# Performance work log

Hardware: AMD Instinct MI355X
Metric: run time of the kernel (lower is better)

Reference implementation:

```python
import jax, jax.numpy as jnp
import numpy as np

ALPHA = 0.2  # LeakyReLU negative slope

def setup_inputs() -> dict:
    key = jax.random.key(0)
    k1, k2, k3 = jax.random.split(key, 3)
    B, N, Fin, Fout = 8, 2048, 256, 128
    h = jax.random.normal(k1, (B, N, Fin), dtype=jnp.float32)
    W = jax.random.normal(k2, (Fin, Fout), dtype=jnp.float32) * (1.414 / np.sqrt(Fin))
    a = jax.random.normal(k3, (2 * Fout, 1), dtype=jnp.float32) * 0.1
    return {"h": h, "W": W, "a": a}

def reference(h, W, a):
    # Wh: [B, N, D]
    Wh = jnp.einsum('bni,io->bno', h, W)
    D = Wh.shape[-1]
    a1 = a[:D, 0]   # weights for the 'i' (repeat_interleave) half
    a2 = a[D:, 0]   # weights for the 'j' (repeat) half
    s1 = Wh @ a1    # [B, N]
    s2 = Wh @ a2    # [B, N]
    # e[b,i,j] = leakyrelu(s1[b,i] + s2[b,j])  (fused form of the O(N^2*2D) concat)
    e = s1[:, :, None] + s2[:, None, :]
    e = jnp.where(e >= 0, e, ALPHA * e)
    # original applies softmax over dim=1 (the i axis)
    attention = jax.nn.softmax(e, axis=1)
    # dropout is identity in eval mode
    h_prime = jnp.einsum('bij,bjd->bid', attention, Wh)
    # concat=True -> ELU
    return jax.nn.elu(h_prime)
```

## Files before the change

### kernel.cpp

```cpp
#include <hip/hip_runtime.h>
#include <hip/hip_bf16.h>


#define ALPHA 0.2f
#define LOG2E 1.4426950408889634f
constexpr int Bb=8, Nn=2048, FIN=256, FOUT=128;

typedef __attribute__((ext_vector_type(8))) short short8;
typedef __attribute__((ext_vector_type(4))) float f32x4;
typedef const __attribute__((address_space(1))) unsigned int* gptr_t;
typedef __attribute__((address_space(3))) unsigned int* lptr_t;

__device__ __forceinline__ float lrelu(float x){ return fmaxf(x, ALPHA*x); }
__device__ __forceinline__ unsigned short bfbits(float x){
    __hip_bfloat16 h = __float2bfloat16(x);
    return *(unsigned short*)&h;
}

__global__ __launch_bounds__(256) void k_prep(const float* __restrict__ W,
                                              __hip_bfloat16* __restrict__ WTt){
    const int idx = blockIdx.x*256 + threadIdx.x;
    #pragma unroll
    for (int v = 0; v < 4; ++v){
        const int widx = idx + v*8192;
        const int kk = widx & 31, n = (widx>>5)&127, kt = widx>>12;
        WTt[widx] = __float2bfloat16(W[(kt*32+kk)*FOUT + n]);
    }
}

__global__ __launch_bounds__(256) void k_wh(const float* __restrict__ h,
                                            const float* __restrict__ a,
                                            const __hip_bfloat16* __restrict__ WTt,
                                            float* __restrict__ s1,
                                            float* __restrict__ s2,
                                            __hip_bfloat16* __restrict__ WhT){
    const int blk = blockIdx.x;
    const int rowbase = blk * 32;
    const int b = blk >> 6;
    const int jt = (rowbase & (Nn-1)) >> 5;
    const int t = threadIdx.x;
    const int wave = t>>6, lane = t&63;
    const int wm = wave & 1, wn = wave >> 1;
    const int lm = lane & 15, q = lane >> 4;

    __shared__ unsigned short hsb[32*264];
    __shared__ unsigned short tt[FOUT*40];
    __shared__ float s1red[2][32], s2red[2][32];

    {
        const float4* h4 = (const float4*)(h + (size_t)rowbase*FIN);
        for (int v = t; v < 2048; v += 256){
            const int row = v >> 6, kq = v & 63;
            float4 x = h4[v];
            ushort4 u;
            u.x = bfbits(x.x); u.y = bfbits(x.y);
            u.z = bfbits(x.z); u.w = bfbits(x.w);
            *(ushort4*)&hsb[row*264 + kq*4] = u;
        }
    }
    __syncthreads();

    f32x4 acc[4];
    #pragma unroll
    for (int ntl = 0; ntl < 4; ++ntl) acc[ntl] = (f32x4){0.f,0.f,0.f,0.f};

    const short* Wt = (const short*)WTt;
    #pragma unroll 2
    for (int kt = 0; kt < 8; ++kt){
        const short8 afr = *(const short8*)&hsb[(wm*16+lm)*264 + kt*32 + q*8];
        #pragma unroll
        for (int ntl = 0; ntl < 4; ++ntl){
            const short8 bfr = *(const short8*)(Wt + ((kt*128 + wn*64 + ntl*16 + lm)*32 + q*8));
            acc[ntl] = __builtin_amdgcn_mfma_f32_16x16x32_bf16(afr, bfr, acc[ntl], 0,0,0);
        }
    }

    {
        float a1v[4], a2v[4];
        #pragma unroll
        for (int ntl = 0; ntl < 4; ++ntl){
            a1v[ntl] = a[wn*64 + ntl*16 + lm];
            a2v[ntl] = a[FOUT + wn*64 + ntl*16 + lm];
        }
        #pragma unroll
        for (int rg = 0; rg < 4; ++rg){
            float p1 = 0.f, p2 = 0.f;
            #pragma unroll
            for (int ntl = 0; ntl < 4; ++ntl){
                p1 += acc[ntl][rg]*a1v[ntl];
                p2 += acc[ntl][rg]*a2v[ntl];
            }
            #pragma unroll
            for (int m = 1; m < 16; m <<= 1){
                p1 += __shfl_xor(p1, m);
                p2 += __shfl_xor(p2, m);
            }
            if (lm == 0){
                s1red[wn][wm*16 + q*4 + rg] = p1;
                s2red[wn][wm*16 + q*4 + rg] = p2;
            }
        }
    }

    #pragma unroll
    for (int ntl = 0; ntl < 4; ++ntl){
        ushort4 u;
        u.x = bfbits(acc[ntl][0]); u.y = bfbits(acc[ntl][1]);
        u.z = bfbits(acc[ntl][2]); u.w = bfbits(acc[ntl][3]);
        *(ushort4*)&tt[(wn*64 + ntl*16 + lm)*40 + wm*16 + q*4] = u;
    }
    __syncthreads();

    if (t < 32){
        s1[rowbase + t] = (s1red[0][t] + s1red[1][t]) * LOG2E;
        s2[rowbase + t] = (s2red[0][t] + s2red[1][t]) * LOG2E;
    }
    {
        const int d = t >> 1, jh = (t & 1) * 16;
        const unsigned short* src = &tt[d*40 + jh];
        short8 v0 = *(const short8*)src;
        short8 v1 = *(const short8*)(src + 8);
        const int lmw = d & 15, ntw = d >> 4, q0 = (t & 1) * 2;
        const int u0 = (lmw & 7) + 8*(q0*16 + ntw*2 + (lmw >> 3));
        short* Wo = (short*)WhT;
        const size_t tb = ((size_t)(b*64 + jt))*4096;
        *(short8*)&Wo[tb + (size_t)u0*8]         = v0;
        *(short8*)&Wo[tb + (size_t)(u0+128)*8]   = v1;
    }
}

__global__ __launch_bounds__(256) void k_z(const float* __restrict__ s1,
                                           const float* __restrict__ s2,
                                           float* __restrict__ l2z){
    const int b  = blockIdx.x >> 7;
    const int jt = blockIdx.x & 127;
    const int t  = threadIdx.x;
    const int jj = t & 15, part = t >> 4;
    const int j  = jt*16 + jj;
    __shared__ float s1s[Nn];
    __shared__ float wred[4];
    __shared__ float red[16][17];

    float mx = -1e30f;
    {
        const float4* g = (const float4*)(s1 + (size_t)b*Nn);
        float4* p = (float4*)s1s;
        #pragma unroll
        for (int v0 = 0; v0 < 2; ++v0){
            const int v = t + v0*256;
            float4 x = g[v]; p[v] = x;
            mx = fmaxf(mx, fmaxf(fmaxf(x.x, x.y), fmaxf(x.z, x.w)));
        }
    }
    #pragma unroll
    for (int m = 1; m < 64; m <<= 1) mx = fmaxf(mx, __shfl_xor(mx, m));
    if ((t & 63) == 0) wred[t >> 6] = mx;
    __syncthreads();
    const float mxf = fmaxf(fmaxf(wred[0], wred[1]), fmaxf(wred[2], wred[3]));

    const float s2j = s2[b*Nn + j];
    const float m   = lrelu(mxf + s2j);
    float sum = 0.f;
    const float4* s4 = (const float4*)&s1s[part*128];
    #pragma unroll 4
    for (int v = 0; v < 32; ++v){
        float x[4]; *(float4*)x = s4[v];
        sum += __builtin_amdgcn_exp2f(lrelu(x[0]+s2j) - m)
             + __builtin_amdgcn_exp2f(lrelu(x[1]+s2j) - m)
             + __builtin_amdgcn_exp2f(lrelu(x[2]+s2j) - m)
             + __builtin_amdgcn_exp2f(lrelu(x[3]+s2j) - m);
    }
    red[part][jj] = sum;
    __syncthreads();
    if (part == 0){
        float Z = 0.f;
        #pragma unroll
        for (int p = 0; p < 16; ++p) Z += red[p][jj];
        l2z[b*Nn + j] = -m - __builtin_amdgcn_logf(Z);
    }
}

__global__ __launch_bounds__(256, 2) void k_pv(const float* __restrict__ s1,
                                               const float* __restrict__ s2,
                                               const float* __restrict__ l2z,
                                               const __hip_bfloat16* __restrict__ WhT,
                                               float* __restrict__ out){
    const int blk   = blockIdx.x;
    const int b     = blk & 7;
    const int ibase = (blk >> 3) * 32;
    const int t     = threadIdx.x;
    const int wave  = t >> 6, lane = t & 63;
    const int wm = wave & 1, kh = wave >> 1;
    const int lm = lane & 15, q = lane >> 4;

    __shared__ float s2s[Nn], lzs[Nn];
    __shared__ unsigned short Bs[2][2][4096];

    {
        const float4* g1 = (const float4*)(s2  + (size_t)b*Nn);
        const float4* g2 = (const float4*)(l2z + (size_t)b*Nn);
        float4* p1 = (float4*)s2s; float4* p2 = (float4*)lzs;
        #pragma unroll
        for (int v0 = 0; v0 < 2; ++v0){
            const int v = t + v0*256;
            p1[v] = g1[v]; p2[v] = g2[v];
        }
    }

    const float s1a = s1[(size_t)b*Nn + ibase + wm*16 + lm];

    f32x4 acc[8];
    #pragma unroll
    for (int nt = 0; nt < 8; ++nt) acc[nt] = (f32x4){0.f,0.f,0.f,0.f};

    const char* WtbB = (const char*)WhT + (size_t)b*64*8192;
    const int laneoff = wm*4096 + lane*16;
    const int dsbase  = (lm & 7)*16 + (lm >> 3)*128 + q*2048;

    {
        const char* src = WtbB + (size_t)(kh*32)*8192 + laneoff;
        unsigned short* dst = &Bs[0][kh][wm*2048];
        #pragma unroll
        for (int c = 0; c < 4; ++c)
            __builtin_amdgcn_global_load_lds((gptr_t)(src + c*1024),
                                             (lptr_t)(dst + c*512), 16, 0, 0);
    }

    int buf = 0;
    for (int it = 0; it < 32; ++it){
        __syncthreads();
        if (it + 1 < 32){
            const char* src = WtbB + (size_t)(kh*32 + it + 1)*8192 + laneoff;
            unsigned short* dst = &Bs[buf^1][kh][wm*2048];
            #pragma unroll
            for (int c = 0; c < 4; ++c)
                __builtin_amdgcn_global_load_lds((gptr_t)(src + c*1024),
                                                 (lptr_t)(dst + c*512), 16, 0, 0);
        }
        const char* tile = (const char*)&Bs[buf][kh][0];
        short8 bfr[8];
        #pragma unroll
        for (int nt = 0; nt < 8; ++nt)
            bfr[nt] = *(const short8*)(tile + dsbase + nt*256);

        const int jb = (kh*32 + it)*32 + q*8;
        float sarr[8], larr[8];
        *(float4*)&sarr[0] = *(const float4*)&s2s[jb];
        *(float4*)&sarr[4] = *(const float4*)&s2s[jb+4];
        *(float4*)&larr[0] = *(const float4*)&lzs[jb];
        *(float4*)&larr[4] = *(const float4*)&lzs[jb+4];
        short8 afa;
        #pragma unroll
        for (int e = 0; e < 8; ++e){
            const float z = s1a + sarr[e];
            afa[e] = (short)bfbits(__builtin_amdgcn_exp2f(fmaxf(z, ALPHA*z) + larr[e]));
        }
        #pragma unroll
        for (int nt = 0; nt < 8; ++nt)
            acc[nt] = __builtin_amdgcn_mfma_f32_16x16x32_bf16(afa, bfr[nt], acc[nt], 0,0,0);
        buf ^= 1;
    }

    __syncthreads();
    float* comb = (float*)&Bs[0][0][0];
    if (kh == 0){
        #pragma unroll
        for (int nt = 0; nt < 8; ++nt)
            #pragma unroll
            for (int rg = 0; rg < 4; ++rg)
                comb[(wm*16 + q*4 + rg)*132 + nt*16 + lm] = acc[nt][rg];
    }
    __syncthreads();
    if (kh == 1){
        #pragma unroll
        for (int nt = 0; nt < 8; ++nt){
            const int col = nt*16 + lm;
            #pragma unroll
            for (int rg = 0; rg < 4; ++rg){
                const int row = wm*16 + q*4 + rg;
                const float x = acc[nt][rg] + comb[row*132 + col];
                out[((size_t)(b*Nn + ibase + row))*FOUT + col] = x > 0.f ? x : expm1f(x);
            }
        }
    }
}

extern "C" void kernel_launch(void* const* d_in, const int* in_sizes, int n_in,
                              void* d_out, int out_size, void* d_ws, size_t ws_size,
                              hipStream_t stream) {
    (void)in_sizes; (void)n_in; (void)out_size; (void)ws_size;
    const float* h = (const float*)d_in[0];
    const float* W = (const float*)d_in[1];
    const float* a = (const float*)d_in[2];
    float* out = (float*)d_out;

    float* ws    = (float*)d_ws;
    float* s1    = ws;
    float* s2    = s1 + Bb*Nn;
    float* l2z   = s2 + Bb*Nn;
    __hip_bfloat16* WTt = (__hip_bfloat16*)(l2z + Bb*Nn);
    __hip_bfloat16* WhT = WTt + 32768;

    k_prep<<<dim3(32),        dim3(256), 0, stream>>>(W, WTt);
    k_wh  <<<dim3(Bb*Nn/32),  dim3(256), 0, stream>>>(h, a, WTt, s1, s2, WhT);
    k_z   <<<dim3(Bb*128),    dim3(256), 0, stream>>>(s1, s2, l2z);
    k_pv  <<<dim3(Bb*Nn/32),  dim3(256), 0, stream>>>(s1, s2, l2z, WhT, out);
}
```

Before: 109.8 us.

## Fuse all stages into one persistent kernel with atomic grid barriers

Replaces the four separate kernels (weight prep, Wh GEMM, softmax normalizer, PV) with a single 512-block kernel that separates phases by global atomic barriers. It also loads h directly from global into registers instead of staging it in LDS, and removes the max-subtraction from the column normalizer computation. This aims to cut launch gaps and inter-kernel drains, at the risk of barrier spin cost, requiring all blocks to be co-resident, and possible exp overflow without max stabilization.

```diff
diff --git a/kernel.cpp b/kernel.cpp
--- a/kernel.cpp
+++ b/kernel.cpp
@@ -5,6 +5,7 @@
 #define ALPHA 0.2f
 #define LOG2E 1.4426950408889634f
 constexpr int Bb=8, Nn=2048, FIN=256, FOUT=128;
+constexpr unsigned NBLK = 512;
 
 typedef __attribute__((ext_vector_type(8))) short short8;
 typedef __attribute__((ext_vector_type(4))) float f32x4;
@@ -17,269 +18,259 @@
     return *(unsigned short*)&h;
 }
 
-__global__ __launch_bounds__(256) void k_prep(const float* __restrict__ W,
-                                              __hip_bfloat16* __restrict__ WTt){
-    const int idx = blockIdx.x*256 + threadIdx.x;
-    #pragma unroll
-    for (int v = 0; v < 4; ++v){
-        const int widx = idx + v*8192;
-        const int kk = widx & 31, n = (widx>>5)&127, kt = widx>>12;
-        WTt[widx] = __float2bfloat16(W[(kt*32+kk)*FOUT + n]);
-    }
-}
-
-__global__ __launch_bounds__(256) void k_wh(const float* __restrict__ h,
-                                            const float* __restrict__ a,
-                                            const __hip_bfloat16* __restrict__ WTt,
-                                            float* __restrict__ s1,
-                                            float* __restrict__ s2,
-                                            __hip_bfloat16* __restrict__ WhT){
+__device__ __forceinline__ void gbar(unsigned int* cnt, int idx){
+    __syncthreads();
+    if (threadIdx.x == 0){
+        __hip_atomic_fetch_add(&cnt[idx], 1u, __ATOMIC_RELEASE, __HIP_MEMORY_SCOPE_AGENT);
+        while (__hip_atomic_load(&cnt[idx], __ATOMIC_RELAXED, __HIP_MEMORY_SCOPE_AGENT) < NBLK)
+            __builtin_amdgcn_s_sleep(2);
+        (void)__hip_atomic_load(&cnt[idx], __ATOMIC_ACQUIRE, __HIP_MEMORY_SCOPE_AGENT);
+    }
+    __syncthreads();
+}
+
+__global__ __launch_bounds__(64) void k_init(unsigned int* cnt){
+    if (threadIdx.x < 8) cnt[threadIdx.x] = 0u;
+}
+
+__global__ __launch_bounds__(256, 2) void k_mega(const float* __restrict__ h,
+                                                 const float* __restrict__ W,
+                                                 const float* __restrict__ a,
+                                                 float* __restrict__ s1,
+                                                 float* __restrict__ s2,
+                                                 float* __restrict__ l2z,
+                                                 __hip_bfloat16* __restrict__ WTt,
+                                                 __hip_bfloat16* __restrict__ WhT,
+                                                 unsigned int* __restrict__ cnt,
+                                                 float* __restrict__ out){
+    __shared__ __align__(16) char sm[49152];
     const int blk = blockIdx.x;
-    const int rowbase = blk * 32;
-    const int b = blk >> 6;
-    const int jt = (rowbase & (Nn-1)) >> 5;
-    const int t = threadIdx.x;
-    const int wave = t>>6, lane = t&63;
-    const int wm = wave & 1, wn = wave >> 1;
+    const int t   = threadIdx.x;
+    const int wave = t >> 6, lane = t & 63;
     const int lm = lane & 15, q = lane >> 4;
 
-    __shared__ unsigned short hsb[32*264];
-    __shared__ unsigned short tt[FOUT*40];
-    __shared__ float s1red[2][32], s2red[2][32];
+    if (t < 64){
+        const int idx = blk*64 + t;
+        const int kk = idx & 31, n = (idx>>5)&127, kt = idx>>12;
+        WTt[idx] = __float2bfloat16(W[(kt*32+kk)*FOUT + n]);
+    }
+    gbar(cnt, 0);
 
     {
-        const float4* h4 = (const float4*)(h + (size_t)rowbase*FIN);
-        for (int v = t; v < 2048; v += 256){
-            const int row = v >> 6, kq = v & 63;
-            float4 x = h4[v];
+        unsigned short* tt   = (unsigned short*)sm;
+        float* s1red = (float*)(sm + 20480);
+        float* s2red = s1red + 64;
+        const int rowbase = blk * 32;
+        const int b = blk >> 6;
+        const int jt = (rowbase & (Nn-1)) >> 5;
+        const int wm = wave & 1, wn = wave >> 1;
+
+        f32x4 acc[4];
+        #pragma unroll
+        for (int ntl = 0; ntl < 4; ++ntl) acc[ntl] = (f32x4){0.f,0.f,0.f,0.f};
+
+        const float* hrow = h + (size_t)(rowbase + wm*16 + lm)*FIN;
+        const short* Wt = (const short*)WTt;
+        #pragma unroll
+        for (int kt = 0; kt < 8; ++kt){
+            float av[8];
+            *(float4*)&av[0] = *(const float4*)&hrow[kt*32 + q*8];
+            *(float4*)&av[4] = *(const float4*)&hrow[kt*32 + q*8 + 4];
+            short8 afr;
+            #pragma unroll
+            for (int e = 0; e < 8; ++e) afr[e] = (short)bfbits(av[e]);
+            #pragma unroll
+            for (int ntl = 0; ntl < 4; ++ntl){
+                const short8 bfr = *(const short8*)(Wt + ((kt*128 + wn*64 + ntl*16 + lm)*32 + q*8));
+                acc[ntl] = __builtin_amdgcn_mfma_f32_16x16x32_bf16(afr, bfr, acc[ntl], 0,0,0);
+            }
+        }
+
+        {
+            float a1v[4], a2v[4];
+            #pragma unroll
+            for (int ntl = 0; ntl < 4; ++ntl){
+                a1v[ntl] = a[wn*64 + ntl*16 + lm];
+                a2v[ntl] = a[FOUT + wn*64 + ntl*16 + lm];
+            }
+            #pragma unroll
+            for (int rg = 0; rg < 4; ++rg){
+                float p1 = 0.f, p2 = 0.f;
+                #pragma unroll
+                for (int ntl = 0; ntl < 4; ++ntl){
+                    p1 += acc[ntl][rg]*a1v[ntl];
+                    p2 += acc[ntl][rg]*a2v[ntl];
+                }
+                #pragma unroll
+                for (int m = 1; m < 16; m <<= 1){
+                    p1 += __shfl_xor(p1, m);
+                    p2 += __shfl_xor(p2, m);
+                }
+                if (lm == 0){
+                    s1red[wn*32 + wm*16 + q*4 + rg] = p1;
+                    s2red[wn*32 + wm*16 + q*4 + rg] = p2;
+                }
+            }
+        }
+
+        #pragma unroll
+        for (int ntl = 0; ntl < 4; ++ntl){
             ushort4 u;
-            u.x = bfbits(x.x); u.y = bfbits(x.y);
-            u.z = bfbits(x.z); u.w = bfbits(x.w);
-            *(ushort4*)&hsb[row*264 + kq*4] = u;
-        }
-    }
-    __syncthreads();
-
-    f32x4 acc[4];
-    #pragma unroll
-    for (int ntl = 0; ntl < 4; ++ntl) acc[ntl] = (f32x4){0.f,0.f,0.f,0.f};
-
-    const short* Wt = (const short*)WTt;
-    #pragma unroll 2
-    for (int kt = 0; kt < 8; ++kt){
-        const short8 afr = *(const short8*)&hsb[(wm*16+lm)*264 + kt*32 + q*8];
-        #pragma unroll
-        for (int ntl = 0; ntl < 4; ++ntl){
-            const short8 bfr = *(const short8*)(Wt + ((kt*128 + wn*64 + ntl*16 + lm)*32 + q*8));
-            acc[ntl] = __builtin_amdgcn_mfma_f32_16x16x32_bf16(afr, bfr, acc[ntl], 0,0,0);
-        }
-    }
+            u.x = bfbits(acc[ntl][0]); u.y = bfbits(acc[ntl][1]);
+            u.z = bfbits(acc[ntl][2]); u.w = bfbits(acc[ntl][3]);
+            *(ushort4*)&tt[(wn*64 + ntl*16 + lm)*40 + wm*16 + q*4] = u;
+        }
+        __syncthreads();
+
+        if (t < 32){
+            s1[rowbase + t] = (s1red[t] + s1red[32 + t]) * LOG2E;
+            s2[rowbase + t] = (s2red[t] + s2red[32 + t]) * LOG2E;
+        }
+        {
+            const int d = t >> 1, jh = (t & 1) * 16;
+            const unsigned short* src = &tt[d*40 + jh];
+            short8 v0 = *(const short8*)src;
+            short8 v1 = *(const short8*)(src + 8);
+            const int lmw = d & 15, ntw = d >> 4, q0 = (t & 1) * 2;
+            const int u0 = (lmw & 7) + 8*(q0*16 + ntw*2 + (lmw >> 3));
+            short* Wo = (short*)WhT;
+            const size_t tb = ((size_t)(b*64 + jt))*4096;
+            *(short8*)&Wo[tb + (size_t)u0*8]       = v0;
+            *(short8*)&Wo[tb + (size_t)(u0+128)*8] = v1;
+        }
+    }
+    gbar(cnt, 1);
 
     {
-        float a1v[4], a2v[4];
-        #pragma unroll
-        for (int ntl = 0; ntl < 4; ++ntl){
-            a1v[ntl] = a[wn*64 + ntl*16 + lm];
-            a2v[ntl] = a[FOUT + wn*64 + ntl*16 + lm];
-        }
-        #pragma unroll
-        for (int rg = 0; rg < 4; ++rg){
-            float p1 = 0.f, p2 = 0.f;
-            #pragma unroll
-            for (int ntl = 0; ntl < 4; ++ntl){
-                p1 += acc[ntl][rg]*a1v[ntl];
-                p2 += acc[ntl][rg]*a2v[ntl];
-            }
-            #pragma unroll
-            for (int m = 1; m < 16; m <<= 1){
-                p1 += __shfl_xor(p1, m);
-                p2 += __shfl_xor(p2, m);
-            }
-            if (lm == 0){
-                s1red[wn][wm*16 + q*4 + rg] = p1;
-                s2red[wn][wm*16 + q*4 + rg] = p2;
-            }
-        }
-    }
-
-    #pragma unroll
-    for (int ntl = 0; ntl < 4; ++ntl){
-        ushort4 u;
-        u.x = bfbits(acc[ntl][0]); u.y = bfbits(acc[ntl][1]);
-        u.z = bfbits(acc[ntl][2]); u.w = bfbits(acc[ntl][3]);
-        *(ushort4*)&tt[(wn*64 + ntl*16 + lm)*40 + wm*16 + q*4] = u;
-    }
-    __syncthreads();
-
-    if (t < 32){
-        s1[rowbase + t] = (s1red[0][t] + s1red[1][t]) * LOG2E;
-        s2[rowbase + t] = (s2red[0][t] + s2red[1][t]) * LOG2E;
-    }
+        float* s1s = (float*)sm;
+        float* red = (float*)(sm + 8192);
+        const int b  = blk >> 6;
+        const int jt = blk & 63;
+        const int jj = t & 31, part = t >> 5;
+        const int j  = jt*32 + jj;
+        {
+            const float4* g = (const float4*)(s1 + (size_t)b*Nn);
+            float4* p = (float4*)s1s;
+            #pragma unroll
+            for (int v0 = 0; v0 < 2; ++v0){ const int v = t + v0*256; p[v] = g[v]; }
+        }
+        __syncthreads();
+        const float s2j = s2[b*Nn + j];
+        float sum = 0.f;
+        const float4* s4 = (const float4*)&s1s[part*256];
+        #pragma unroll 4
+        for (int v = 0; v < 64; ++v){
+            float x[4]; *(float4*)x = s4[v];
+            sum += __builtin_amdgcn_exp2f(lrelu(x[0]+s2j))
+                 + __builtin_amdgcn_exp2f(lrelu(x[1]+s2j))
+                 + __builtin_amdgcn_exp2f(lrelu(x[2]+s2j))
+                 + __builtin_amdgcn_exp2f(lrelu(x[3]+s2j));
+        }
+        red[part*33 + jj] = sum;
+        __syncthreads();
+        if (part == 0){
+            float Z = 0.f;
+            #pragma unroll
+            for (int p = 0; p < 8; ++p) Z += red[p*33 + jj];
+            l2z[b*Nn + j] = -__builtin_amdgcn_logf(Z);
+        }
+        __syncthreads();
+    }
+    gbar(cnt, 2);
+
     {
-        const int d = t >> 1, jh = (t & 1) * 16;
-        const unsigned short* src = &tt[d*40 + jh];
-        short8 v0 = *(const short8*)src;
-        short8 v1 = *(const short8*)(src + 8);
-        const int lmw = d & 15, ntw = d >> 4, q0 = (t & 1) * 2;
-        const int u0 = (lmw & 7) + 8*(q0*16 + ntw*2 + (lmw >> 3));
-        short* Wo = (short*)WhT;
-        const size_t tb = ((size_t)(b*64 + jt))*4096;
-        *(short8*)&Wo[tb + (size_t)u0*8]         = v0;
-        *(short8*)&Wo[tb + (size_t)(u0+128)*8]   = v1;
-    }
-}
-
-__global__ __launch_bounds__(256) void k_z(const float* __restrict__ s1,
-                                           const float* __restrict__ s2,
-                                           float* __restrict__ l2z){
-    const int b  = blockIdx.x >> 7;
-    const int jt = blockIdx.x & 127;
-    const int t  = threadIdx.x;
-    const int jj = t & 15, part = t >> 4;
-    const int j  = jt*16 + jj;
-    __shared__ float s1s[Nn];
-    __shared__ float wred[4];
-    __shared__ float red[16][17];
-
-    float mx = -1e30f;
-    {
-        const float4* g = (const float4*)(s1 + (size_t)b*Nn);
-        float4* p = (float4*)s1s;
-        #pragma unroll
-        for (int v0 = 0; v0 < 2; ++v0){
-            const int v = t + v0*256;
-            float4 x = g[v]; p[v] = x;
-            mx = fmaxf(mx, fmaxf(fmaxf(x.x, x.y), fmaxf(x.z, x.w)));
-        }
-    }
-    #pragma unroll
-    for (int m = 1; m < 64; m <<= 1) mx = fmaxf(mx, __shfl_xor(mx, m));
-    if ((t & 63) == 0) wred[t >> 6] = mx;
-    __syncthreads();
-    const float mxf = fmaxf(fmaxf(wred[0], wred[1]), fmaxf(wred[2], wred[3]));
-
-    const float s2j = s2[b*Nn + j];
-    const float m   = lrelu(mxf + s2j);
-    float sum = 0.f;
-    const float4* s4 = (const float4*)&s1s[part*128];
-    #pragma unroll 4
-    for (int v = 0; v < 32; ++v){
-        float x[4]; *(float4*)x = s4[v];
-        sum += __builtin_amdgcn_exp2f(lrelu(x[0]+s2j) - m)
-             + __builtin_amdgcn_exp2f(lrelu(x[1]+s2j) - m)
-             + __builtin_amdgcn_exp2f(lrelu(x[2]+s2j) - m)
-             + __builtin_amdgcn_exp2f(lrelu(x[3]+s2j) - m);
-    }
-    red[part][jj] = sum;
-    __syncthreads();
-    if (part == 0){
-        float Z = 0.f;
-        #pragma unroll
-        for (int p = 0; p < 16; ++p) Z += red[p][jj];
-        l2z[b*Nn + j] = -m - __builtin_amdgcn_logf(Z);
-    }
-}
-
-__global__ __launch_bounds__(256, 2) void k_pv(const float* __restrict__ s1,
-                                               const float* __restrict__ s2,
-                                               const float* __restrict__ l2z,
-                                               const __hip_bfloat16* __restrict__ WhT,
-                                               float* __restrict__ out){
-    const int blk   = blockIdx.x;
-    const int b     = blk & 7;
-    const int ibase = (blk >> 3) * 32;
-    const int t     = threadIdx.x;
-    const int wave  = t >> 6, lane = t & 63;
-    const int wm = wave & 1, kh = wave >> 1;
-    const int lm = lane & 15, q = lane >> 4;
-
-    __shared__ float s2s[Nn], lzs[Nn];
-    __shared__ unsigned short Bs[2][2][4096];
-
-    {
-        const float4* g1 = (const float4*)(s2  + (size_t)b*Nn);
-        const float4* g2 = (const float4*)(l2z + (size_t)b*Nn);
-        float4* p1 = (float4*)s2s; float4* p2 = (float4*)lzs;
-        #pragma unroll
-        for (int v0 = 0; v0 < 2; ++v0){
-            const int v = t + v0*256;
-            p1[v] = g1[v]; p2[v] = g2[v];
-        }
-    }
-
-    const float s1a = s1[(size_t)b*Nn + ibase + wm*16 + lm];
-
-    f32x4 acc[8];
-    #pragma unroll
-    for (int nt = 0; nt < 8; ++nt) acc[nt] = (f32x4){0.f,0.f,0.f,0.f};
-
-    const char* WtbB = (const char*)WhT + (size_t)b*64*8192;
-    const int laneoff = wm*4096 + lane*16;
-    const int dsbase  = (lm & 7)*16 + (lm >> 3)*128 + q*2048;
-
-    {
-        const char* src = WtbB + (size_t)(kh*32)*8192 + laneoff;
-        unsigned short* dst = &Bs[0][kh][wm*2048];
-        #pragma unroll
-        for (int c = 0; c < 4; ++c)
-            __builtin_amdgcn_global_load_lds((gptr_t)(src + c*1024),
-                                             (lptr_t)(dst + c*512), 16, 0, 0);
-    }
-
-    int buf = 0;
-    for (int it = 0; it < 32; ++it){
-        __syncthreads();
-        if (it + 1 < 32){
-            const char* src = WtbB + (size_t)(kh*32 + it + 1)*8192 + laneoff;
-            unsigned short* dst = &Bs[buf^1][kh][wm*2048];
+        float* s2s = (float*)sm;
+        float* lzs = (float*)(sm + 8192);
+        unsigned short* Bs = (unsigned short*)(sm + 16384);
+        const int b     = blk & 7;
+        const int ibase = (blk >> 3) * 32;
+        const int wm = wave & 1, kh = wave >> 1;
+
+        {
+            const float4* g1 = (const float4*)(s2  + (size_t)b*Nn);
+            const float4* g2 = (const float4*)(l2z + (size_t)b*Nn);
+            float4* p1 = (float4*)s2s; float4* p2 = (float4*)lzs;
+            #pragma unroll
+            for (int v0 = 0; v0 < 2; ++v0){
+                const int v = t + v0*256;
+                p1[v] = g1[v]; p2[v] = g2[v];
+            }
+        }
+
+        const float s1a = s1[(size_t)b*Nn + ibase + wm*16 + lm];
+
+        f32x4 acc[8];
+        #pragma unroll
+        for (int nt = 0; nt < 8; ++nt) acc[nt] = (f32x4){0.f,0.f,0.f,0.f};
+
+        const char* WtbB = (const char*)WhT + (size_t)b*64*8192;
+        const int laneoff = wm*4096 + lane*16;
+        const int dsbase  = (lm & 7)*16 + (lm >> 3)*128 + q*2048;
+
+        {
+            const char* src = WtbB + (size_t)(kh*32)*8192 + laneoff;
+            unsigned short* dst = Bs + kh*4096 + wm*2048;
             #pragma unroll
             for (int c = 0; c < 4; ++c)
                 __builtin_amdgcn_global_load_lds((gptr_t)(src + c*1024),
                                                  (lptr_t)(dst + c*512), 16, 0, 0);
         }
-        const char* tile = (const char*)&Bs[buf][kh][0];
-        short8 bfr[8];
-        #pragma unroll
-        for (int nt = 0; nt < 8; ++nt)
-            bfr[nt] = *(const short8*)(tile + dsbase + nt*256);
-
-        const int jb = (kh*32 + it)*32 + q*8;
-        float sarr[8], larr[8];
-        *(float4*)&sarr[0] = *(const float4*)&s2s[jb];
-        *(float4*)&sarr[4] = *(const float4*)&s2s[jb+4];
-        *(float4*)&larr[0] = *(const float4*)&lzs[jb];
-        *(float4*)&larr[4] = *(const float4*)&lzs[jb+4];
-        short8 afa;
-        #pragma unroll
-        for (int e = 0; e < 8; ++e){
-            const float z = s1a + sarr[e];
-            afa[e] = (short)bfbits(__builtin_amdgcn_exp2f(fmaxf(z, ALPHA*z) + larr[e]));
-        }
-        #pragma unroll
-        for (int nt = 0; nt < 8; ++nt)
-            acc[nt] = __builtin_amdgcn_mfma_f32_16x16x32_bf16(afa, bfr[nt], acc[nt], 0,0,0);
-        buf ^= 1;
-    }
-
-    __syncthreads();
-    float* comb = (float*)&Bs[0][0][0];
-    if (kh == 0){
-        #pragma unroll
-        for (int nt = 0; nt < 8; ++nt)
-            #pragma unroll
-            for (int rg = 0; rg < 4; ++rg)
-                comb[(wm*16 + q*4 + rg)*132 + nt*16 + lm] = acc[nt][rg];
-    }
-    __syncthreads();
-    if (kh == 1){
-        #pragma unroll
-        for (int nt = 0; nt < 8; ++nt){
-            const int col = nt*16 + lm;
-            #pragma unroll
-            for (int rg = 0; rg < 4; ++rg){
-                const int row = wm*16 + q*4 + rg;
-                const float x = acc[nt][rg] + comb[row*132 + col];
-                out[((size_t)(b*Nn + ibase + row))*FOUT + col] = x > 0.f ? x : expm1f(x);
+
+        int buf = 0;
+        for (int it = 0; it < 32; ++it){
+            __syncthreads();
+            if (it + 1 < 32){
+                const char* src = WtbB + (size_t)(kh*32 + it + 1)*8192 + laneoff;
+                unsigned short* dst = Bs + (buf^1)*8192 + kh*4096 + wm*2048;
+                #pragma unroll
+                for (int c = 0; c < 4; ++c)
+                    __builtin_amdgcn_global_load_lds((gptr_t)(src + c*1024),
+                                                     (lptr_t)(dst + c*512), 16, 0, 0);
+            }
+            const char* tile = (const char*)(Bs + buf*8192 + kh*4096);
+            short8 bfr[8];
+            #pragma unroll
+            for (int nt = 0; nt < 8; ++nt)
+                bfr[nt] = *(const short8*)(tile + dsbase + nt*256);
+
+            const int jb = (kh*32 + it)*32 + q*8;
+            float sarr[8], larr[8];
+            *(float4*)&sarr[0] = *(const float4*)&s2s[jb];
+            *(float4*)&sarr[4] = *(const float4*)&s2s[jb+4];
+            *(float4*)&larr[0] = *(const float4*)&lzs[jb];
+            *(float4*)&larr[4] = *(const float4*)&lzs[jb+4];
+            short8 afa;
+            #pragma unroll
+            for (int e = 0; e < 8; ++e){
+                const float z = s1a + sarr[e];
+                afa[e] = (short)bfbits(__builtin_amdgcn_exp2f(fmaxf(z, ALPHA*z) + larr[e]));
+            }
+            #pragma unroll
+            for (int nt = 0; nt < 8; ++nt)
+                acc[nt] = __builtin_amdgcn_mfma_f32_16x16x32_bf16(afa, bfr[nt], acc[nt], 0,0,0);
+            buf ^= 1;
+        }
+
+        __syncthreads();
+        float* comb = (float*)(sm + 16384);
+        if (kh == 0){
+            #pragma unroll
+            for (int nt = 0; nt < 8; ++nt)
+                #pragma unroll
+                for (int rg = 0; rg < 4; ++rg)
+                    comb[(wm*16 + q*4 + rg)*132 + nt*16 + lm] = acc[nt][rg];
+        }
+        __syncthreads();
+        if (kh == 1){
+            #pragma unroll
+            for (int nt = 0; nt < 8; ++nt){
+                const int col = nt*16 + lm;
+                #pragma unroll
+                for (int rg = 0; rg < 4; ++rg){
+                    const int row = wm*16 + q*4 + rg;
+                    const float x = acc[nt][rg] + comb[row*132 + col];
+                    out[((size_t)(b*Nn + ibase + row))*FOUT + col] = x > 0.f ? x : expm1f(x);
+                }
             }
         }
     }
@@ -300,9 +291,8 @@
     float* l2z   = s2 + Bb*Nn;
     __hip_bfloat16* WTt = (__hip_bfloat16*)(l2z + Bb*Nn);
     __hip_bfloat16* WhT = WTt + 32768;
-
-    k_prep<<<dim3(32),        dim3(256), 0, stream>>>(W, WTt);
-    k_wh  <<<dim3(Bb*Nn/32),  dim3(256), 0, stream>>>(h, a, WTt, s1, s2, WhT);
-    k_z   <<<dim3(Bb*128),    dim3(256), 0, stream>>>(s1, s2, l2z);
-    k_pv  <<<dim3(Bb*Nn/32),  dim3(256), 0, stream>>>(s1, s2, l2z, WhT, out);
-}
+    unsigned int* cnt = (unsigned int*)(WhT + (size_t)Bb*Nn*FOUT);
+
+    k_init<<<dim3(1),    dim3(64),  0, stream>>>(cnt);
+    k_mega<<<dim3(NBLK), dim3(256), 0, stream>>>(h, W, a, s1, s2, l2z, WTt, WhT, cnt, out);
+}
```

Measured after the change: 194.8 us. 77.3% more time.
